# Kernel tuning notes

Hardware: AMD Instinct MI355X
Metric: run time of the kernel (lower is better)

The kernel has to match this reference:

```python
import jax, jax.numpy as jnp
import numpy as np

DIM = 512      # model dim
HEADS = 8
DH = DIM // HEADS          # 64, dim_head
M = DIM // 2               # 256, num_landmarks
ITERS = 6                  # pinv_iterations
K = 33                     # residual_conv_kernel (lucidrains default)
B, N = 4, 4096             # N divisible by M -> no padding branch


def setup_inputs() -> dict:
    key = jax.random.key(0)
    ks = jax.random.split(key, 5)
    s = 0.02
    return {
        "x": jax.random.normal(ks[0], (B, N, DIM), jnp.float32),
        "ln_w": jnp.ones((DIM,), jnp.float32),
        "ln_b": jnp.zeros((DIM,), jnp.float32),
        "w_qkv": jax.random.normal(ks[1], (DIM, 3 * HEADS * DH), jnp.float32) * s,
        "w_out": jax.random.normal(ks[2], (HEADS * DH, DIM), jnp.float32) * s,
        "b_out": jnp.zeros((DIM,), jnp.float32),
        "w_conv": jax.random.normal(ks[3], (HEADS, 1, K, 1), jnp.float32) * s,  # depthwise Conv2d (h,1,33,1)
    }


def _moore_penrose_pinv(x, iters=ITERS):
    # Newton-Schulz iterative pseudo-inverse, as in lucidrains nystrom-attention
    abs_x = jnp.abs(x)
    col = abs_x.sum(-1)
    row = abs_x.sum(-2)
    z = jnp.swapaxes(x, -1, -2) / (jnp.max(col) * jnp.max(row))  # global max, matching torch.max
    I = jnp.eye(x.shape[-1], dtype=x.dtype)
    for _ in range(iters):
        xz = x @ z
        z = 0.25 * z @ (13.0 * I - xz @ (15.0 * I - xz @ (7.0 * I - xz)))
    return z


def reference(x, ln_w, ln_b, w_qkv, w_out, b_out, w_conv):
    b, n, d = x.shape
    # LayerNorm (biased variance, eps=1e-5 as torch default)
    mu = jnp.mean(x, -1, keepdims=True)
    var = jnp.mean(jnp.square(x - mu), -1, keepdims=True)
    xn = (x - mu) / jnp.sqrt(var + 1e-5) * ln_w + ln_b

    qkv = xn @ w_qkv                                   # [b,n,3*h*dh]
    q, k, v = jnp.split(qkv, 3, axis=-1)
    split = lambda t: t.reshape(b, n, HEADS, DH).transpose(0, 2, 1, 3)  # [b,h,n,dh]
    q, k, v = split(q), split(k), split(v)
    q = q * (DH ** -0.5)

    l = n // M                                         # tokens per landmark
    q_l = q.reshape(b, HEADS, M, l, DH).mean(axis=3)   # [b,h,m,dh]
    k_l = k.reshape(b, HEADS, M, l, DH).mean(axis=3)

    sim1 = jnp.einsum('bhid,bhjd->bhij', q, k_l)       # [b,h,n,m]
    sim2 = jnp.einsum('bhid,bhjd->bhij', q_l, k_l)     # [b,h,m,m]
    sim3 = jnp.einsum('bhid,bhjd->bhij', q_l, k)       # [b,h,m,n]
    a1 = jax.nn.softmax(sim1, -1)
    a2 = jax.nn.softmax(sim2, -1)
    a3 = jax.nn.softmax(sim3, -1)

    a2_inv = _moore_penrose_pinv(a2)
    out = (a1 @ a2_inv) @ (a3 @ v)                     # [b,h,n,dh]

    # depthwise residual conv over sequence dim (kernel (33,1), groups=heads)
    res = jax.lax.conv_general_dilated(
        v, w_conv, window_strides=(1, 1),
        padding=((K // 2, K // 2), (0, 0)),
        dimension_numbers=('NCHW', 'OIHW', 'NCHW'),
        feature_group_count=HEADS)
    out = out + res

    out = out.transpose(0, 2, 1, 3).reshape(b, n, HEADS * DH)
    out = out @ w_out + b_out
    return x + out
```

## Files before the change

### kernel.cpp

```cpp
#include <hip/hip_runtime.h>
#include <cstdint>

typedef __bf16 bf16;
typedef __bf16 bf16x8 __attribute__((ext_vector_type(8)));
typedef float  f32x4  __attribute__((ext_vector_type(4)));

__global__ __launch_bounds__(256) void prep_w(const float* __restrict__ wqkv, const float* __restrict__ wout,
                                              bf16* __restrict__ wqkvT, bf16* __restrict__ woutT) {
  int idx = blockIdx.x * 256 + threadIdx.x;
  if (idx < 98304) {
    int r8 = idx & 63, c = idx >> 6;
    bf16 o[8];
#pragma unroll
    for (int e = 0; e < 8; e++) o[e] = (bf16)wqkv[(long)(r8 * 8 + e) * 1536 + c];
    *(uint4*)(wqkvT + (long)c * 512 + r8 * 8) = *(uint4*)o;
  } else {
    int j = idx - 98304;
    int r8 = j & 63, c = j >> 6;
    bf16 o[8];
#pragma unroll
    for (int e = 0; e < 8; e++) o[e] = (bf16)wout[(long)(r8 * 8 + e) * 512 + c];
    *(uint4*)(woutT + (long)c * 512 + r8 * 8) = *(uint4*)o;
  }
}

__global__ __launch_bounds__(64) void ln_kernel(const float* __restrict__ x,
    const float* __restrict__ w, const float* __restrict__ b, bf16* __restrict__ xn) {
  long row = blockIdx.x;
  int t = threadIdx.x;
  const float* rp = x + row * 512 + t * 8;
  float4 p0 = *(const float4*)rp;
  float4 p1 = *(const float4*)(rp + 4);
  float vals[8] = {p0.x, p0.y, p0.z, p0.w, p1.x, p1.y, p1.z, p1.w};
  float s = 0.f, s2 = 0.f;
#pragma unroll
  for (int e = 0; e < 8; e++) { s += vals[e]; s2 += vals[e] * vals[e]; }
#pragma unroll
  for (int o = 32; o > 0; o >>= 1) { s += __shfl_xor(s, o); s2 += __shfl_xor(s2, o); }
  float mu = s * (1.f / 512.f);
  float var = s2 * (1.f / 512.f) - mu * mu;
  float rstd = rsqrtf(var + 1e-5f);
  float4 w0 = *(const float4*)(w + t * 8), w1 = *(const float4*)(w + t * 8 + 4);
  float4 b0 = *(const float4*)(b + t * 8), b1 = *(const float4*)(b + t * 8 + 4);
  float wv[8] = {w0.x, w0.y, w0.z, w0.w, w1.x, w1.y, w1.z, w1.w};
  float bv[8] = {b0.x, b0.y, b0.z, b0.w, b1.x, b1.y, b1.z, b1.w};
  bf16 outv[8];
#pragma unroll
  for (int e = 0; e < 8; e++) outv[e] = (bf16)((vals[e] - mu) * rstd * wv[e] + bv[e]);
  *(uint4*)(xn + row * 512 + t * 8) = *(uint4*)outv;
}

enum { MODE_BF16 = 1, MODE_QKV = 2, MODE_RESID = 3, MODE_XZ = 4, MODE_DIAG = 5, MODE_Y0 = 6, MODE_ZY = 7 };

template <int BM, int BN, bool BT, int MODE>
__global__ __launch_bounds__(256) void gemm_k(
    const bf16* __restrict__ A, const bf16* __restrict__ B, void* __restrict__ C,
    int M, int N, int K, long sA, long sB, long sC, float alpha, float cdiag,
    const float* __restrict__ resid, const float* __restrict__ bias,
    bf16* __restrict__ aux0, bf16* __restrict__ aux1, bf16* __restrict__ aux2) {
  constexpr int BK = 32, LDST = 40;
  __shared__ __align__(16) bf16 As[BM * LDST];
  __shared__ __align__(16) bf16 Bs[BN * LDST];
  const int tid = threadIdx.x, lane = tid & 63, wave = tid >> 6;
  const int quad = lane >> 4, l16 = lane & 15;
  constexpr int WN = (BN >= 128) ? 2 : 1;
  constexpr int WM = 4 / WN;
  constexpr int TM = BM / (WM * 16), TN = BN / (WN * 16);
  const int wm0 = (wave / WN) * (BM / WM);
  const int wn0 = (wave % WN) * (BN / WN);
  const int bm0 = blockIdx.x * BM, bn0 = blockIdx.y * BN;
  const bf16* Ab = A + (long)blockIdx.z * sA;
  const bf16* Bb = B + (long)(MODE == MODE_ZY ? (blockIdx.z & 31) : blockIdx.z) * sB;

  f32x4 zero = {0.f, 0.f, 0.f, 0.f};
  f32x4 acc[TM][TN];
#pragma unroll
  for (int i = 0; i < TM; i++)
#pragma unroll
    for (int j = 0; j < TN; j++) acc[i][j] = zero;

  for (int k0 = 0; k0 < K; k0 += BK) {
    for (int c = tid; c < BM * 4; c += 256) {
      int r = c >> 2, cv = (c & 3) * 8;
      *(uint4*)&As[r * LDST + cv] = *(const uint4*)&Ab[(long)(bm0 + r) * K + k0 + cv];
    }
    if (BT) {
      for (int c = tid; c < BN * 4; c += 256) {
        int r = c >> 2, cv = (c & 3) * 8;
        *(uint4*)&Bs[r * LDST + cv] = *(const uint4*)&Bb[(long)(bn0 + r) * K + k0 + cv];
      }
    } else {
      for (int c = tid; c < BN * 4; c += 256) {
        int kk = c / (BN / 8), nv = (c % (BN / 8)) * 8;
        uint4 tmp = *(const uint4*)&Bb[(long)(k0 + kk) * N + bn0 + nv];
        const bf16* tv = (const bf16*)&tmp;
#pragma unroll
        for (int e = 0; e < 8; e++) Bs[(nv + e) * LDST + kk] = tv[e];
      }
    }
    __syncthreads();
    bf16x8 af[TM], bfr[TN];
#pragma unroll
    for (int i = 0; i < TM; i++)
      af[i] = *(const bf16x8*)&As[(wm0 + i * 16 + l16) * LDST + quad * 8];
#pragma unroll
    for (int j = 0; j < TN; j++)
      bfr[j] = *(const bf16x8*)&Bs[(wn0 + j * 16 + l16) * LDST + quad * 8];
#pragma unroll
    for (int i = 0; i < TM; i++)
#pragma unroll
      for (int j = 0; j < TN; j++)
        acc[i][j] = __builtin_amdgcn_mfma_f32_16x16x32_bf16(af[i], bfr[j], acc[i][j], 0, 0, 0);
    __syncthreads();
  }

  const long cb = (long)blockIdx.z * sC;
  float rscale = 1.f;
  if (MODE == MODE_Y0) rscale = 1.f / (resid[0] * resid[1]);
#pragma unroll
  for (int i = 0; i < TM; i++)
#pragma unroll
    for (int j = 0; j < TN; j++)
#pragma unroll
      for (int r = 0; r < 4; r++) {
        int row = bm0 + wm0 + i * 16 + quad * 4 + r;
        int col = bn0 + wn0 + j * 16 + l16;
        float v = acc[i][j][r] * alpha;
        if (MODE == MODE_BF16) {
          ((bf16*)C)[cb + (long)row * N + col] = (bf16)v;
        } else if (MODE == MODE_QKV) {
          int b = row >> 12, n = row & 4095;
          int which = col >> 9, h = (col >> 6) & 7, d = col & 63;
          long o = ((long)(b * 8 + h) * 4096 + n) * 64 + d;
          if (which == 0) aux0[o] = (bf16)(v * 0.125f);
          else if (which == 1) aux1[o] = (bf16)v;
          else aux2[o] = (bf16)v;
        } else if (MODE == MODE_Y0) {
          long o = cb + (long)row * N + col;
          float vv = v * rscale;
          aux0[o] = (bf16)vv;
          aux1[o] = (bf16)(((row == col) ? cdiag : 0.f) - vv);
        } else if (MODE == MODE_ZY) {
          long o = cb + (long)row * N + col;
          ((bf16*)C)[o] = (bf16)v;
          if (blockIdx.z >= 32) aux1[o - 2097152] = (bf16)(((row == col) ? cdiag : 0.f) - v);
        } else if (MODE == MODE_DIAG) {
          ((bf16*)C)[cb + (long)row * N + col] = (bf16)(((row == col) ? cdiag : 0.f) - v);
        } else {
          long o = (long)row * N + col;
          ((float*)C)[o] = v + bias[col] + resid[o];
        }
      }
}

__global__ __launch_bounds__(256) void lm_kernel(const bf16* __restrict__ q, const bf16* __restrict__ k,
                                                 bf16* __restrict__ ql, bf16* __restrict__ kl) {
  int bh = blockIdx.x, mi = blockIdx.y * 4 + (threadIdx.x >> 6), d = threadIdx.x & 63;
  long base = ((long)bh * 4096 + mi * 16) * 64 + d;
  float sq = 0.f, sk = 0.f;
#pragma unroll
  for (int j = 0; j < 16; j++) { sq += (float)q[base + j * 64]; sk += (float)k[base + j * 64]; }
  long o = ((long)bh * 256 + mi) * 64 + d;
  ql[o] = (bf16)(sq * (1.f / 16.f));
  kl[o] = (bf16)(sk * (1.f / 16.f));
}

__global__ __launch_bounds__(256) void softmax256(bf16* __restrict__ buf) {
  long row = blockIdx.x;
  int t = threadIdx.x, lane = t & 63, wave = t >> 6;
  __shared__ float sm[4];
  float v = (float)buf[row * 256 + t];
  float m = v;
#pragma unroll
  for (int o = 32; o > 0; o >>= 1) m = fmaxf(m, __shfl_xor(m, o));
  if (lane == 0) sm[wave] = m;
  __syncthreads();
  m = fmaxf(fmaxf(sm[0], sm[1]), fmaxf(sm[2], sm[3]));
  float e = __expf(v - m);
  __syncthreads();
  float s = e;
#pragma unroll
  for (int o = 32; o > 0; o >>= 1) s += __shfl_xor(s, o);
  if (lane == 0) sm[wave] = s;
  __syncthreads();
  s = sm[0] + sm[1] + sm[2] + sm[3];
  buf[row * 256 + t] = (bf16)(e / s);
}

__global__ void init_scal(float* scal) { scal[0] = 1.0f; ((int*)scal)[1] = 0; }

__global__ __launch_bounds__(64) void red_col(const bf16* __restrict__ a2h, float* scal) {
  int bh = blockIdx.x;
  int j = blockIdx.y * 64 + threadIdx.x;
  float s = 0.f;
  const bf16* p = a2h + (long)bh * 65536 + j;
  for (int i = 0; i < 256; i++) s += (float)p[i * 256];
  atomicMax((int*)scal + 1, __float_as_int(s));
}

__global__ __launch_bounds__(256) void z0_k(const bf16* __restrict__ a2h,
                                            const float* __restrict__ scal, bf16* __restrict__ z) {
  int bh = blockIdx.x, i = blockIdx.y, j = threadIdx.x;
  float inv = 1.f / (scal[0] * scal[1]);
  float v = (float)a2h[((long)bh * 256 + i) * 256 + j];
  z[((long)bh * 256 + j) * 256 + i] = (bf16)(v * inv);
}

__global__ __launch_bounds__(256) void wt_k(const bf16* __restrict__ W, bf16* __restrict__ WT) {
  int bh = blockIdx.x, tid = threadIdx.x;
  const bf16* wb = W + (long)bh * 16384;
  bf16* wtb = WT + (long)bh * 16384;
  for (int i = tid; i < 2048; i += 256) {
    int n = i >> 3, d8 = (i & 7) * 8;
    uint4 pk = *(const uint4*)&wb[n * 64 + d8];
    const bf16* pv = (const bf16*)&pk;
#pragma unroll
    for (int e = 0; e < 8; e++) wtb[(d8 + e) * 256 + n] = pv[e];
  }
}

__global__ __launch_bounds__(256) void f3_partial(const bf16* __restrict__ ql,
    const bf16* __restrict__ k, const bf16* __restrict__ v,
    float* __restrict__ Opart, float* __restrict__ lpart) {
  const int mt = blockIdx.x, ns = blockIdx.y, bh = blockIdx.z;
  const int tid = threadIdx.x, lane = tid & 63, wave = tid >> 6;
  const int quad = lane >> 4, l16 = lane & 15;
  const int wr0 = mt * 128 + wave * 32;
  __shared__ __align__(16) bf16 vT[64][72];
  __shared__ __align__(16) bf16 Pts[4][32][72];

  const bf16* qlb = ql + (long)bh * 16384;
  const bf16* kb  = k + (long)bh * 262144;
  const bf16* vb  = v + (long)bh * 262144;

  bf16x8 aq[2][2];
#pragma unroll
  for (int ti = 0; ti < 2; ti++)
#pragma unroll
    for (int ki = 0; ki < 2; ki++)
      aq[ti][ki] = *(const bf16x8*)&qlb[(wr0 + ti * 16 + l16) * 64 + ki * 32 + quad * 8];

  f32x4 zero = {0.f, 0.f, 0.f, 0.f};
  f32x4 Oacc[2][4];
#pragma unroll
  for (int i = 0; i < 2; i++)
#pragma unroll
    for (int j = 0; j < 4; j++) Oacc[i][j] = zero;
  float lacc[2][4] = {};

  for (int c = 0; c < 8; c++) {
    int n0c = ns * 512 + c * 64;
    __syncthreads();
    for (int i = tid; i < 512; i += 256) {
      int nn = i >> 3, d8 = (i & 7) * 8;
      uint4 pk = *(const uint4*)&vb[(long)(n0c + nn) * 64 + d8];
      const bf16* pv = (const bf16*)&pk;
#pragma unroll
      for (int e = 0; e < 8; e++) vT[d8 + e][nn] = pv[e];
    }
    __syncthreads();

    f32x4 sacc[2][4];
#pragma unroll
    for (int i = 0; i < 2; i++)
#pragma unroll
      for (int j = 0; j < 4; j++) sacc[i][j] = zero;
#pragma unroll
    for (int ki = 0; ki < 2; ki++) {
      bf16x8 bk[4];
#pragma unroll
      for (int tj = 0; tj < 4; tj++)
        bk[tj] = *(const bf16x8*)&kb[(long)(n0c + tj * 16 + l16) * 64 + ki * 32 + quad * 8];
#pragma unroll
      for (int ti = 0; ti < 2; ti++)
#pragma unroll
        for (int tj = 0; tj < 4; tj++)
          sacc[ti][tj] = __builtin_amdgcn_mfma_f32_16x16x32_bf16(aq[ti][ki], bk[tj], sacc[ti][tj], 0, 0, 0);
    }
#pragma unroll
    for (int ti = 0; ti < 2; ti++)
#pragma unroll
      for (int tj = 0; tj < 4; tj++)
#pragma unroll
        for (int r = 0; r < 4; r++) {
          float e = __expf(sacc[ti][tj][r]);
          lacc[ti][r] += e;
          Pts[wave][ti * 16 + quad * 4 + r][tj * 16 + l16] = (bf16)e;
        }
#pragma unroll
    for (int ki = 0; ki < 2; ki++) {
      bf16x8 ap[2], bv[4];
#pragma unroll
      for (int ti = 0; ti < 2; ti++)
        ap[ti] = *(const bf16x8*)&Pts[wave][ti * 16 + l16][ki * 32 + quad * 8];
#pragma unroll
      for (int tj = 0; tj < 4; tj++)
        bv[tj] = *(const bf16x8*)&vT[tj * 16 + l16][ki * 32 + quad * 8];
#pragma unroll
      for (int ti = 0; ti < 2; ti++)
#pragma unroll
        for (int tj = 0; tj < 4; tj++)
          Oacc[ti][tj] = __builtin_amdgcn_mfma_f32_16x16x32_bf16(ap[ti], bv[tj], Oacc[ti][tj], 0, 0, 0);
    }
  }

#pragma unroll
  for (int ti = 0; ti < 2; ti++)
#pragma unroll
    for (int r = 0; r < 4; r++) {
#pragma unroll
      for (int o = 1; o < 16; o <<= 1) lacc[ti][r] += __shfl_xor(lacc[ti][r], o);
    }
  long pb = ((long)bh * 8 + ns) * 256;
#pragma unroll
  for (int ti = 0; ti < 2; ti++)
#pragma unroll
    for (int r = 0; r < 4; r++) {
      int row = wr0 + ti * 16 + quad * 4 + r;
      if (l16 == 0) lpart[pb + row] = lacc[ti][r];
#pragma unroll
      for (int tj = 0; tj < 4; tj++)
        Opart[(pb + row) * 64 + tj * 16 + l16] = Oacc[ti][tj][r];
    }
}

__global__ __launch_bounds__(256) void f3_combine(const float* __restrict__ Opart,
    const float* __restrict__ lpart, bf16* __restrict__ a3v) {
  int row = blockIdx.x * 4 + (threadIdx.x >> 6);
  int d = threadIdx.x & 63;
  int bh = row >> 8, m = row & 255;
  float so = 0.f, sl = 0.f;
#pragma unroll
  for (int s = 0; s < 8; s++) {
    long pb = ((long)bh * 8 + s) * 256 + m;
    so += Opart[pb * 64 + d];
    sl += lpart[pb];
  }
  a3v[(long)row * 64 + d] = (bf16)(so / sl);
}

__global__ __launch_bounds__(256) void f1_attn(const bf16* __restrict__ q,
    const bf16* __restrict__ kl, const bf16* __restrict__ WT, const bf16* __restrict__ v,
    const float* __restrict__ wconv, bf16* __restrict__ xattn) {
  const int nt = blockIdx.x, bh = blockIdx.y;
  const int h = bh & 7, b = bh >> 3, n0 = nt * 64;
  const int tid = threadIdx.x, lane = tid & 63, wave = tid >> 6;
  const int quad = lane >> 4, l16 = lane & 15;
  __shared__ __align__(16) bf16 Pts[64][264];
  __shared__ __align__(16) bf16 vsT[64][104];
  __shared__ float red[4][64];
  __shared__ float linv[64];

  const bf16* qb  = q + (long)bh * 262144;
  const bf16* klb = kl + (long)bh * 16384;
  const bf16* wtb = WT + (long)bh * 16384;
  const bf16* vb  = v + (long)bh * 262144;

  float wreg = (lane < 33) ? wconv[h * 33 + lane] : 0.f;

  for (int i = tid; i < 768; i += 256) {
    int r = i >> 3, d8 = (i & 7) * 8;
    int n = n0 - 16 + r;
    uint4 val = {0u, 0u, 0u, 0u};
    if (n >= 0 && n < 4096) val = *(const uint4*)&vb[(long)n * 64 + d8];
    const bf16* pv = (const bf16*)&val;
#pragma unroll
    for (int e = 0; e < 8; e++) vsT[d8 + e][r] = pv[e];
  }

  f32x4 zero = {0.f, 0.f, 0.f, 0.f};
  f32x4 sacc[4][4];
#pragma unroll
  for (int i = 0; i < 4; i++)
#pragma unroll
    for (int j = 0; j < 4; j++) sacc[i][j] = zero;
#pragma unroll
  for (int ki = 0; ki < 2; ki++) {
    bf16x8 aq[4], bk[4];
#pragma unroll
    for (int ti = 0; ti < 4; ti++)
      aq[ti] = *(const bf16x8*)&qb[(long)(n0 + ti * 16 + l16) * 64 + ki * 32 + quad * 8];
#pragma unroll
    for (int tj = 0; tj < 4; tj++)
      bk[tj] = *(const bf16x8*)&klb[(long)(wave * 64 + tj * 16 + l16) * 64 + ki * 32 + quad * 8];
#pragma unroll
    for (int ti = 0; ti < 4; ti++)
#pragma unroll
      for (int tj = 0; tj < 4; tj++)
        sacc[ti][tj] = __builtin_amdgcn_mfma_f32_16x16x32_bf16(aq[ti], bk[tj], sacc[ti][tj], 0, 0, 0);
  }
  float ps[4][4] = {};
#pragma unroll
  for (int ti = 0; ti < 4; ti++)
#pragma unroll
    for (int tj = 0; tj < 4; tj++)
#pragma unroll
      for (int r = 0; r < 4; r++) {
        float e = __expf(sacc[ti][tj][r]);
        ps[ti][r] += e;
        Pts[ti * 16 + quad * 4 + r][wave * 64 + tj * 16 + l16] = (bf16)e;
      }
#pragma unroll
  for (int ti = 0; ti < 4; ti++)
#pragma unroll
    for (int r = 0; r < 4; r++) {
#pragma unroll
      for (int o = 1; o < 16; o <<= 1) ps[ti][r] += __shfl_xor(ps[ti][r], o);
      if (l16 == 0) red[wave][ti * 16 + quad * 4 + r] = ps[ti][r];
    }
  __syncthreads();
  if (tid < 64) linv[tid] = 1.f / (red[0][tid] + red[1][tid] + red[2][tid] + red[3][tid]);
  __syncthreads();

  const int r0 = wave * 16;
  f32x4 Oacc[4];
#pragma unroll
  for (int j = 0; j < 4; j++) Oacc[j] = zero;
#pragma unroll
  for (int ki = 0; ki < 8; ki++) {
    bf16x8 ap = *(const bf16x8*)&Pts[r0 + l16][ki * 32 + quad * 8];
    bf16x8 bw[4];
#pragma unroll
    for (int tj = 0; tj < 4; tj++)
      bw[tj] = *(const bf16x8*)&wtb[(long)(tj * 16 + l16) * 256 + ki * 32 + quad * 8];
#pragma unroll
    for (int tj = 0; tj < 4; tj++)
      Oacc[tj] = __builtin_amdgcn_mfma_f32_16x16x32_bf16(ap, bw[tj], Oacc[tj], 0, 0, 0);
  }

  f32x4 Cacc[4];
#pragma unroll
  for (int j = 0; j < 4; j++) Cacc[j] = zero;
#pragma unroll
  for (int ki = 0; ki < 3; ki++) {
    if (ki * 32 + 31 < r0 || ki * 32 > r0 + 47) continue;
    bf16x8 av;
#pragma unroll
    for (int j = 0; j < 8; j++) {
      int idx = ki * 32 + quad * 8 + j - r0 - l16;
      float wv = __shfl(wreg, idx & 63);
      av[j] = (idx >= 0 && idx < 33) ? (bf16)wv : (bf16)0.f;
    }
    bf16x8 bv[4];
#pragma unroll
    for (int tj = 0; tj < 4; tj++)
      bv[tj] = *(const bf16x8*)&vsT[tj * 16 + l16][ki * 32 + quad * 8];
#pragma unroll
    for (int tj = 0; tj < 4; tj++)
      Cacc[tj] = __builtin_amdgcn_mfma_f32_16x16x32_bf16(av, bv[tj], Cacc[tj], 0, 0, 0);
  }

#pragma unroll
  for (int rr = 0; rr < 4; rr++) {
    int row = r0 + quad * 4 + rr;
    float inv = linv[row];
    int n = n0 + row;
#pragma unroll
    for (int tj = 0; tj < 4; tj++) {
      int d = tj * 16 + l16;
      xattn[(((long)b * 4096 + n) << 9) + (h << 6) + d] = (bf16)(Oacc[tj][rr] * inv + Cacc[tj][rr]);
    }
  }
}

extern "C" void kernel_launch(void* const* d_in, const int* in_sizes, int n_in,
                              void* d_out, int out_size, void* d_ws, size_t ws_size,
                              hipStream_t stream) {
  (void)in_sizes; (void)n_in; (void)out_size; (void)ws_size;
  const float* x      = (const float*)d_in[0];
  const float* ln_w   = (const float*)d_in[1];
  const float* ln_b   = (const float*)d_in[2];
  const float* w_qkv  = (const float*)d_in[3];
  const float* w_out  = (const float*)d_in[4];
  const float* b_out  = (const float*)d_in[5];
  const float* w_conv = (const float*)d_in[6];
  float* out = (float*)d_out;

  char* ws = (char*)d_ws;
  const size_t MB = 1u << 20;
  bf16* q      = (bf16*)(ws + 0 * MB);
  bf16* k      = (bf16*)(ws + 16 * MB);
  bf16* v      = (bf16*)(ws + 32 * MB);
  bf16* xn     = (bf16*)(ws + 48 * MB);
  bf16* a2_h   = (bf16*)(ws + 48 * MB);
  bf16* pbuf   = (bf16*)(ws + 52 * MB);
  bf16* qbuf   = (bf16*)(ws + 56 * MB);
  bf16* rbuf   = (bf16*)(ws + 60 * MB);
  bf16* bufA   = (bf16*)(ws + 64 * MB);
  bf16* bufB   = (bf16*)(ws + 72 * MB);
  float* Opart = (float*)(ws + 48 * MB);
  float* lpart = (float*)(ws + 72 * MB);
  bf16* xattn  = (bf16*)(ws + 73 * MB);
  bf16* wqkvT  = (bf16*)(ws + 73 * MB);
  bf16* ql     = (bf16*)(ws + 89 * MB);
  bf16* kl     = (bf16*)(ws + 90 * MB);
  bf16* a3v    = (bf16*)(ws + 91 * MB);
  bf16* W      = (bf16*)(ws + 92 * MB);
  bf16* WT     = (bf16*)(ws + 93 * MB);
  bf16* woutT  = (bf16*)(ws + 94 * MB);
  float* scal  = (float*)(ws + 94 * MB + 512 * 1024);

  prep_w<<<512, 256, 0, stream>>>(w_qkv, w_out, wqkvT, woutT);

  ln_kernel<<<16384, 64, 0, stream>>>(x, ln_w, ln_b, xn);

  gemm_k<128, 128, true, MODE_QKV><<<dim3(128, 12, 1), 256, 0, stream>>>(
      xn, wqkvT, nullptr, 16384, 1536, 512, 0, 0, 0, 1.f, 0.f, nullptr, nullptr, q, k, v);

  lm_kernel<<<dim3(32, 64), 256, 0, stream>>>(q, k, ql, kl);

  gemm_k<64, 64, true, MODE_BF16><<<dim3(4, 4, 32), 256, 0, stream>>>(
      ql, kl, a2_h, 256, 256, 64, 16384, 16384, 65536, 1.f, 0.f, nullptr, nullptr, nullptr, nullptr, nullptr);
  softmax256<<<8192, 256, 0, stream>>>(a2_h);

  init_scal<<<1, 1, 0, stream>>>(scal);
  red_col<<<dim3(32, 4), 64, 0, stream>>>(a2_h, scal);
  z0_k<<<dim3(32, 256), 256, 0, stream>>>(a2_h, scal, bufA);
  gemm_k<64, 64, true, MODE_Y0><<<dim3(4, 4, 32), 256, 0, stream>>>(
      a2_h, a2_h, nullptr, 256, 256, 256, 65536, 65536, 65536, 1.f, 7.f, scal, nullptr,
      bufA + 2097152, pbuf, nullptr);

  bf16* cur = bufA;
  bf16* nxt = bufB;
  for (int it = 0; it < 6; it++) {
    gemm_k<64, 64, true, MODE_DIAG><<<dim3(4, 4, 32), 256, 0, stream>>>(
        cur + 2097152, pbuf, qbuf, 256, 256, 256, 65536, 65536, 65536, 1.f, 15.f,
        nullptr, nullptr, nullptr, nullptr, nullptr);
    gemm_k<64, 64, true, MODE_DIAG><<<dim3(4, 4, 32), 256, 0, stream>>>(
        cur + 2097152, qbuf, rbuf, 256, 256, 256, 65536, 65536, 65536, 1.f, 13.f,
        nullptr, nullptr, nullptr, nullptr, nullptr);
    if (it < 5) {
      gemm_k<64, 64, true, MODE_ZY><<<dim3(4, 4, 64), 256, 0, stream>>>(
          cur, rbuf, nxt, 256, 256, 256, 65536, 65536, 65536, 0.25f, 7.f,
          nullptr, nullptr, nullptr, pbuf, nullptr);
    } else {
      gemm_k<64, 64, true, MODE_BF16><<<dim3(4, 4, 32), 256, 0, stream>>>(
          cur, rbuf, nxt, 256, 256, 256, 65536, 65536, 65536, 0.25f, 0.f,
          nullptr, nullptr, nullptr, nullptr, nullptr);
    }
    bf16* tmp = cur; cur = nxt; nxt = tmp;
  }

  f3_partial<<<dim3(2, 8, 32), 256, 0, stream>>>(ql, k, v, Opart, lpart);
  f3_combine<<<2048, 256, 0, stream>>>(Opart, lpart, a3v);

  gemm_k<64, 64, false, MODE_BF16><<<dim3(4, 1, 32), 256, 0, stream>>>(
      cur, a3v, W, 256, 64, 256, 65536, 16384, 16384, 1.f, 0.f, nullptr, nullptr, nullptr, nullptr, nullptr);
  wt_k<<<32, 256, 0, stream>>>(W, WT);

  f1_attn<<<dim3(64, 32), 256, 0, stream>>>(q, kl, WT, v, w_conv, xattn);

  gemm_k<128, 128, true, MODE_RESID><<<dim3(128, 4, 1), 256, 0, stream>>>(
      xattn, woutT, out, 16384, 512, 512, 0, 0, 0, 1.f, 0.f, x, b_out, nullptr, nullptr, nullptr);
}
```

Baseline: 489.8 us.

## Use direct global-to-LDS loads in GEMMs and alias LDS in f1_attn

Adds a new GEMM kernel that stages A and B tiles with global_load_lds 16-byte transfers into unpadded LDS, skipping the register round-trip, and routes every BT GEMM through it. The old gemm_k is kept only for the non-transposed W product. In f1_attn the depthwise-conv MFMA moves ahead of the score computation, so the v tile buffer can share LDS with the P buffer. Launch bounds are raised to 4 blocks per CU to improve occupancy. The unpadded LDS layout may introduce bank conflicts on the fragment reads.

```diff
diff --git a/kernel.cpp b/kernel.cpp
--- a/kernel.cpp
+++ b/kernel.cpp
@@ -4,6 +4,11 @@
 typedef __bf16 bf16;
 typedef __bf16 bf16x8 __attribute__((ext_vector_type(8)));
 typedef float  f32x4  __attribute__((ext_vector_type(4)));
+
+__device__ __forceinline__ void glds16(const void* g, void* l) {
+  __builtin_amdgcn_global_load_lds((const __attribute__((address_space(1))) void*)g,
+                                   (__attribute__((address_space(3))) void*)l, 16, 0, 0);
+}
 
 __global__ __launch_bounds__(256) void prep_w(const float* __restrict__ wqkv, const float* __restrict__ wout,
                                               bf16* __restrict__ wqkvT, bf16* __restrict__ woutT) {
@@ -52,25 +57,27 @@
 
 enum { MODE_BF16 = 1, MODE_QKV = 2, MODE_RESID = 3, MODE_XZ = 4, MODE_DIAG = 5, MODE_Y0 = 6, MODE_ZY = 7 };
 
-template <int BM, int BN, bool BT, int MODE>
-__global__ __launch_bounds__(256) void gemm_k(
+template <int BM, int MODE>
+__global__ __launch_bounds__(256) void gemm_g(
     const bf16* __restrict__ A, const bf16* __restrict__ B, void* __restrict__ C,
-    int M, int N, int K, long sA, long sB, long sC, float alpha, float cdiag,
+    int N, int K, long sA, long sB, long sC, float alpha, float cdiag,
     const float* __restrict__ resid, const float* __restrict__ bias,
     bf16* __restrict__ aux0, bf16* __restrict__ aux1, bf16* __restrict__ aux2) {
-  constexpr int BK = 32, LDST = 40;
-  __shared__ __align__(16) bf16 As[BM * LDST];
-  __shared__ __align__(16) bf16 Bs[BN * LDST];
+  constexpr int BK = 32, BN = BM;
+  __shared__ __align__(16) bf16 As[BM * BK];
+  __shared__ __align__(16) bf16 Bs[BN * BK];
   const int tid = threadIdx.x, lane = tid & 63, wave = tid >> 6;
   const int quad = lane >> 4, l16 = lane & 15;
   constexpr int WN = (BN >= 128) ? 2 : 1;
   constexpr int WM = 4 / WN;
   constexpr int TM = BM / (WM * 16), TN = BN / (WN * 16);
+  constexpr int ISS = BM / 64;
   const int wm0 = (wave / WN) * (BM / WM);
   const int wn0 = (wave % WN) * (BN / WN);
   const int bm0 = blockIdx.x * BM, bn0 = blockIdx.y * BN;
   const bf16* Ab = A + (long)blockIdx.z * sA;
   const bf16* Bb = B + (long)(MODE == MODE_ZY ? (blockIdx.z & 31) : blockIdx.z) * sB;
+  const int srow = lane >> 2, scol = (lane & 3) * 8;
 
   f32x4 zero = {0.f, 0.f, 0.f, 0.f};
   f32x4 acc[TM][TN];
@@ -80,32 +87,20 @@
     for (int j = 0; j < TN; j++) acc[i][j] = zero;
 
   for (int k0 = 0; k0 < K; k0 += BK) {
-    for (int c = tid; c < BM * 4; c += 256) {
-      int r = c >> 2, cv = (c & 3) * 8;
-      *(uint4*)&As[r * LDST + cv] = *(const uint4*)&Ab[(long)(bm0 + r) * K + k0 + cv];
-    }
-    if (BT) {
-      for (int c = tid; c < BN * 4; c += 256) {
-        int r = c >> 2, cv = (c & 3) * 8;
-        *(uint4*)&Bs[r * LDST + cv] = *(const uint4*)&Bb[(long)(bn0 + r) * K + k0 + cv];
-      }
-    } else {
-      for (int c = tid; c < BN * 4; c += 256) {
-        int kk = c / (BN / 8), nv = (c % (BN / 8)) * 8;
-        uint4 tmp = *(const uint4*)&Bb[(long)(k0 + kk) * N + bn0 + nv];
-        const bf16* tv = (const bf16*)&tmp;
-#pragma unroll
-        for (int e = 0; e < 8; e++) Bs[(nv + e) * LDST + kk] = tv[e];
-      }
+#pragma unroll
+    for (int t = 0; t < ISS; t++) {
+      int seg = wave * ISS + t;
+      glds16(&Ab[(long)(bm0 + seg * 16 + srow) * K + k0 + scol], &As[seg * 512]);
+      glds16(&Bb[(long)(bn0 + seg * 16 + srow) * K + k0 + scol], &Bs[seg * 512]);
     }
     __syncthreads();
     bf16x8 af[TM], bfr[TN];
 #pragma unroll
     for (int i = 0; i < TM; i++)
-      af[i] = *(const bf16x8*)&As[(wm0 + i * 16 + l16) * LDST + quad * 8];
+      af[i] = *(const bf16x8*)&As[(wm0 + i * 16 + l16) * BK + quad * 8];
 #pragma unroll
     for (int j = 0; j < TN; j++)
-      bfr[j] = *(const bf16x8*)&Bs[(wn0 + j * 16 + l16) * LDST + quad * 8];
+      bfr[j] = *(const bf16x8*)&Bs[(wn0 + j * 16 + l16) * BK + quad * 8];
 #pragma unroll
     for (int i = 0; i < TM; i++)
 #pragma unroll
@@ -153,6 +148,89 @@
       }
 }
 
+template <int BM, int BN, bool BT, int MODE>
+__global__ __launch_bounds__(256) void gemm_k(
+    const bf16* __restrict__ A, const bf16* __restrict__ B, void* __restrict__ C,
+    int M, int N, int K, long sA, long sB, long sC, float alpha, float cdiag,
+    const float* __restrict__ resid, const float* __restrict__ bias,
+    bf16* __restrict__ aux0, bf16* __restrict__ aux1, bf16* __restrict__ aux2) {
+  constexpr int BK = 32, LDST = 40;
+  __shared__ __align__(16) bf16 As[BM * LDST];
+  __shared__ __align__(16) bf16 Bs[BN * LDST];
+  const int tid = threadIdx.x, lane = tid & 63, wave = tid >> 6;
+  const int quad = lane >> 4, l16 = lane & 15;
+  constexpr int WN = (BN >= 128) ? 2 : 1;
+  constexpr int WM = 4 / WN;
+  constexpr int TM = BM / (WM * 16), TN = BN / (WN * 16);
+  const int wm0 = (wave / WN) * (BM / WM);
+  const int wn0 = (wave % WN) * (BN / WN);
+  const int bm0 = blockIdx.x * BM, bn0 = blockIdx.y * BN;
+  const bf16* Ab = A + (long)blockIdx.z * sA;
+  const bf16* Bb = B + (long)blockIdx.z * sB;
+
+  f32x4 zero = {0.f, 0.f, 0.f, 0.f};
+  f32x4 acc[TM][TN];
+#pragma unroll
+  for (int i = 0; i < TM; i++)
+#pragma unroll
+    for (int j = 0; j < TN; j++) acc[i][j] = zero;
+
+  for (int k0 = 0; k0 < K; k0 += BK) {
+    for (int c = tid; c < BM * 4; c += 256) {
+      int r = c >> 2, cv = (c & 3) * 8;
+      *(uint4*)&As[r * LDST + cv] = *(const uint4*)&Ab[(long)(bm0 + r) * K + k0 + cv];
+    }
+    if (BT) {
+      for (int c = tid; c < BN * 4; c += 256) {
+        int r = c >> 2, cv = (c & 3) * 8;
+        *(uint4*)&Bs[r * LDST + cv] = *(const uint4*)&Bb[(long)(bn0 + r) * K + k0 + cv];
+      }
+    } else {
+      for (int c = tid; c < BN * 4; c += 256) {
+        int kk = c / (BN / 8), nv = (c % (BN / 8)) * 8;
+        uint4 tmp = *(const uint4*)&Bb[(long)(k0 + kk) * N + bn0 + nv];
+        const bf16* tv = (const bf16*)&tmp;
+#pragma unroll
+        for (int e = 0; e < 8; e++) Bs[(nv + e) * LDST + kk] = tv[e];
+      }
+    }
+    __syncthreads();
+    bf16x8 af[TM], bfr[TN];
+#pragma unroll
+    for (int i = 0; i < TM; i++)
+      af[i] = *(const bf16x8*)&As[(wm0 + i * 16 + l16) * LDST + quad * 8];
+#pragma unroll
+    for (int j = 0; j < TN; j++)
+      bfr[j] = *(const bf16x8*)&Bs[(wn0 + j * 16 + l16) * LDST + quad * 8];
+#pragma unroll
+    for (int i = 0; i < TM; i++)
+#pragma unroll
+      for (int j = 0; j < TN; j++)
+        acc[i][j] = __builtin_amdgcn_mfma_f32_16x16x32_bf16(af[i], bfr[j], acc[i][j], 0, 0, 0);
+    __syncthreads();
+  }
+
+  const long cb = (long)blockIdx.z * sC;
+#pragma unroll
+  for (int i = 0; i < TM; i++)
+#pragma unroll
+    for (int j = 0; j < TN; j++)
+#pragma unroll
+      for (int r = 0; r < 4; r++) {
+        int row = bm0 + wm0 + i * 16 + quad * 4 + r;
+        int col = bn0 + wn0 + j * 16 + l16;
+        float v = acc[i][j][r] * alpha;
+        if (MODE == MODE_BF16) {
+          ((bf16*)C)[cb + (long)row * N + col] = (bf16)v;
+        } else if (MODE == MODE_DIAG) {
+          ((bf16*)C)[cb + (long)row * N + col] = (bf16)(((row == col) ? cdiag : 0.f) - v);
+        } else {
+          long o = (long)row * N + col;
+          ((float*)C)[o] = v + bias[col] + resid[o];
+        }
+      }
+}
+
 __global__ __launch_bounds__(256) void lm_kernel(const bf16* __restrict__ q, const bf16* __restrict__ k,
                                                  bf16* __restrict__ ql, bf16* __restrict__ kl) {
   int bh = blockIdx.x, mi = blockIdx.y * 4 + (threadIdx.x >> 6), d = threadIdx.x & 63;
@@ -339,17 +417,18 @@
   a3v[(long)row * 64 + d] = (bf16)(so / sl);
 }
 
-__global__ __launch_bounds__(256) void f1_attn(const bf16* __restrict__ q,
+__global__ __launch_bounds__(256, 4) void f1_attn(const bf16* __restrict__ q,
     const bf16* __restrict__ kl, const bf16* __restrict__ WT, const bf16* __restrict__ v,
     const float* __restrict__ wconv, bf16* __restrict__ xattn) {
   const int nt = blockIdx.x, bh = blockIdx.y;
   const int h = bh & 7, b = bh >> 3, n0 = nt * 64;
   const int tid = threadIdx.x, lane = tid & 63, wave = tid >> 6;
   const int quad = lane >> 4, l16 = lane & 15;
-  __shared__ __align__(16) bf16 Pts[64][264];
-  __shared__ __align__(16) bf16 vsT[64][104];
+  __shared__ __align__(16) bf16 PtsBuf[64 * 264];
   __shared__ float red[4][64];
   __shared__ float linv[64];
+  bf16 (*Pts)[264] = (bf16(*)[264])PtsBuf;
+  bf16 (*vsT)[104] = (bf16(*)[104])PtsBuf;
 
   const bf16* qb  = q + (long)bh * 262144;
   const bf16* klb = kl + (long)bh * 16384;
@@ -367,8 +446,33 @@
 #pragma unroll
     for (int e = 0; e < 8; e++) vsT[d8 + e][r] = pv[e];
   }
+  __syncthreads();
 
   f32x4 zero = {0.f, 0.f, 0.f, 0.f};
+
+  const int r0 = wave * 16;
+  f32x4 Cacc[4];
+#pragma unroll
+  for (int j = 0; j < 4; j++) Cacc[j] = zero;
+#pragma unroll
+  for (int ki = 0; ki < 3; ki++) {
+    if (ki * 32 + 31 < r0 || ki * 32 > r0 + 47) continue;
+    bf16x8 av;
+#pragma unroll
+    for (int j = 0; j < 8; j++) {
+      int idx = ki * 32 + quad * 8 + j - r0 - l16;
+      float wv = __shfl(wreg, idx & 63);
+      av[j] = (idx >= 0 && idx < 33) ? (bf16)wv : (bf16)0.f;
+    }
+    bf16x8 bv[4];
+#pragma unroll
+    for (int tj = 0; tj < 4; tj++)
+      bv[tj] = *(const bf16x8*)&vsT[tj * 16 + l16][ki * 32 + quad * 8];
+#pragma unroll
+    for (int tj = 0; tj < 4; tj++)
+      Cacc[tj] = __builtin_amdgcn_mfma_f32_16x16x32_bf16(av, bv[tj], Cacc[tj], 0, 0, 0);
+  }
+
   f32x4 sacc[4][4];
 #pragma unroll
   for (int i = 0; i < 4; i++)
@@ -389,6 +493,8 @@
       for (int tj = 0; tj < 4; tj++)
         sacc[ti][tj] = __builtin_amdgcn_mfma_f32_16x16x32_bf16(aq[ti], bk[tj], sacc[ti][tj], 0, 0, 0);
   }
+  __syncthreads();
+
   float ps[4][4] = {};
 #pragma unroll
   for (int ti = 0; ti < 4; ti++)
@@ -412,7 +518,6 @@
   if (tid < 64) linv[tid] = 1.f / (red[0][tid] + red[1][tid] + red[2][tid] + red[3][tid]);
   __syncthreads();
 
-  const int r0 = wave * 16;
   f32x4 Oacc[4];
 #pragma unroll
   for (int j = 0; j < 4; j++) Oacc[j] = zero;
@@ -426,28 +531,6 @@
 #pragma unroll
     for (int tj = 0; tj < 4; tj++)
       Oacc[tj] = __builtin_amdgcn_mfma_f32_16x16x32_bf16(ap, bw[tj], Oacc[tj], 0, 0, 0);
-  }
-
-  f32x4 Cacc[4];
-#pragma unroll
-  for (int j = 0; j < 4; j++) Cacc[j] = zero;
-#pragma unroll
-  for (int ki = 0; ki < 3; ki++) {
-    if (ki * 32 + 31 < r0 || ki * 32 > r0 + 47) continue;
-    bf16x8 av;
-#pragma unroll
-    for (int j = 0; j < 8; j++) {
-      int idx = ki * 32 + quad * 8 + j - r0 - l16;
-      float wv = __shfl(wreg, idx & 63);
-      av[j] = (idx >= 0 && idx < 33) ? (bf16)wv : (bf16)0.f;
-    }
-    bf16x8 bv[4];
-#pragma unroll
-    for (int tj = 0; tj < 4; tj++)
-      bv[tj] = *(const bf16x8*)&vsT[tj * 16 + l16][ki * 32 + quad * 8];
-#pragma unroll
-    for (int tj = 0; tj < 4; tj++)
-      Cacc[tj] = __builtin_amdgcn_mfma_f32_16x16x32_bf16(av, bv[tj], Cacc[tj], 0, 0, 0);
   }
 
 #pragma unroll
@@ -501,41 +584,40 @@
   float* scal  = (float*)(ws + 94 * MB + 512 * 1024);
 
   prep_w<<<512, 256, 0, stream>>>(w_qkv, w_out, wqkvT, woutT);
-
   ln_kernel<<<16384, 64, 0, stream>>>(x, ln_w, ln_b, xn);
 
-  gemm_k<128, 128, true, MODE_QKV><<<dim3(128, 12, 1), 256, 0, stream>>>(
-      xn, wqkvT, nullptr, 16384, 1536, 512, 0, 0, 0, 1.f, 0.f, nullptr, nullptr, q, k, v);
+  gemm_g<128, MODE_QKV><<<dim3(128, 12, 1), 256, 0, stream>>>(
+      xn, wqkvT, nullptr, 1536, 512, 0, 0, 0, 1.f, 0.f, nullptr, nullptr, q, k, v);
 
   lm_kernel<<<dim3(32, 64), 256, 0, stream>>>(q, k, ql, kl);
 
-  gemm_k<64, 64, true, MODE_BF16><<<dim3(4, 4, 32), 256, 0, stream>>>(
-      ql, kl, a2_h, 256, 256, 64, 16384, 16384, 65536, 1.f, 0.f, nullptr, nullptr, nullptr, nullptr, nullptr);
+  gemm_g<64, MODE_BF16><<<dim3(4, 4, 32), 256, 0, stream>>>(
+      ql, kl, a2_h, 256, 64, 16384, 16384, 65536, 1.f, 0.f, nullptr, nullptr, nullptr, nullptr, nullptr);
   softmax256<<<8192, 256, 0, stream>>>(a2_h);
 
   init_scal<<<1, 1, 0, stream>>>(scal);
   red_col<<<dim3(32, 4), 64, 0, stream>>>(a2_h, scal);
   z0_k<<<dim3(32, 256), 256, 0, stream>>>(a2_h, scal, bufA);
-  gemm_k<64, 64, true, MODE_Y0><<<dim3(4, 4, 32), 256, 0, stream>>>(
-      a2_h, a2_h, nullptr, 256, 256, 256, 65536, 65536, 65536, 1.f, 7.f, scal, nullptr,
+  gemm_g<64, MODE_Y0><<<dim3(4, 4, 32), 256, 0, stream>>>(
+      a2_h, a2_h, nullptr, 256, 256, 65536, 65536, 65536, 1.f, 7.f, scal, nullptr,
       bufA + 2097152, pbuf, nullptr);
 
   bf16* cur = bufA;
   bf16* nxt = bufB;
   for (int it = 0; it < 6; it++) {
-    gemm_k<64, 64, true, MODE_DIAG><<<dim3(4, 4, 32), 256, 0, stream>>>(
-        cur + 2097152, pbuf, qbuf, 256, 256, 256, 65536, 65536, 65536, 1.f, 15.f,
+    gemm_g<64, MODE_DIAG><<<dim3(4, 4, 32), 256, 0, stream>>>(
+        cur + 2097152, pbuf, qbuf, 256, 256, 65536, 65536, 65536, 1.f, 15.f,
         nullptr, nullptr, nullptr, nullptr, nullptr);
-    gemm_k<64, 64, true, MODE_DIAG><<<dim3(4, 4, 32), 256, 0, stream>>>(
-        cur + 2097152, qbuf, rbuf, 256, 256, 256, 65536, 65536, 65536, 1.f, 13.f,
+    gemm_g<64, MODE_DIAG><<<dim3(4, 4, 32), 256, 0, stream>>>(
+        cur + 2097152, qbuf, rbuf, 256, 256, 65536, 65536, 65536, 1.f, 13.f,
         nullptr, nullptr, nullptr, nullptr, nullptr);
     if (it < 5) {
-      gemm_k<64, 64, true, MODE_ZY><<<dim3(4, 4, 64), 256, 0, stream>>>(
-          cur, rbuf, nxt, 256, 256, 256, 65536, 65536, 65536, 0.25f, 7.f,
+      gemm_g<64, MODE_ZY><<<dim3(4, 4, 64), 256, 0, stream>>>(
+          cur, rbuf, nxt, 256, 256, 65536, 65536, 65536, 0.25f, 7.f,
           nullptr, nullptr, nullptr, pbuf, nullptr);
     } else {
-      gemm_k<64, 64, true, MODE_BF16><<<dim3(4, 4, 32), 256, 0, stream>>>(
-          cur, rbuf, nxt, 256, 256, 256, 65536, 65536, 65536, 0.25f, 0.f,
+      gemm_g<64, MODE_BF16><<<dim3(4, 4, 32), 256, 0, stream>>>(
+          cur, rbuf, nxt, 256, 256, 65536, 65536, 65536, 0.25f, 0.f,
           nullptr, nullptr, nullptr, nullptr, nullptr);
     }
     bf16* tmp = cur; cur = nxt; nxt = tmp;
@@ -550,6 +632,6 @@
 
   f1_attn<<<dim3(64, 32), 256, 0, stream>>>(q, kl, WT, v, w_conv, xattn);
 
-  gemm_k<128, 128, true, MODE_RESID><<<dim3(128, 4, 1), 256, 0, stream>>>(
-      xattn, woutT, out, 16384, 512, 512, 0, 0, 0, 1.f, 0.f, x, b_out, nullptr, nullptr, nullptr);
-}
+  gemm_g<128, MODE_RESID><<<dim3(128, 4, 1), 256, 0, stream>>>(
+      xattn, woutT, out, 512, 512, 0, 0, 0, 1.f, 0.f, x, b_out, nullptr, nullptr, nullptr);
+}
```

Result: no change. 487.1 us (-0.6%).
